# Optimization experiments

Hardware: AMD Instinct MI355X
Metric: run time of the kernel (lower is better)

## Reference

```python
import jax, jax.numpy as jnp
import numpy as np
import math

IN_CH, OUT_CH, RANK, MODES, HEAD, BATCH = 64, 64, 8, 8192, 4, 32


def setup_inputs() -> dict:
    key = jax.random.key(0)
    kx, k1, k2, k3 = jax.random.split(key, 4)
    scale = 1.0 / math.sqrt(IN_CH * OUT_CH)
    x = jax.random.normal(kx, (BATCH, IN_CH, MODES), dtype=jnp.float32)
    # Note: in the torch module, self.U1 has in_channels rows and is used as the
    # FIRST contraction ('irkh'), while self.U2 has out_channels rows and is the
    # LAST ('oskh') — the jit'd function's arg names are swapped relative to the
    # module attributes. We name params by their role here.
    U_in = scale * jax.random.uniform(k1, (IN_CH, RANK, MODES, HEAD), dtype=jnp.float32)   # self.U1
    M = scale * jax.random.uniform(k2, (RANK, RANK, MODES, HEAD), dtype=jnp.float32)       # self.M
    U_out = scale * jax.random.uniform(k3, (OUT_CH, RANK, MODES, HEAD), dtype=jnp.float32) # self.U2
    return {"x": x, "U_in": U_in, "M": M, "U_out": U_out}


def reference(x, U_in, M, U_out):
    # x: [b, i, k] -> r: [b, r, k, h]
    r = jnp.einsum('irkh,bik->brkh', U_in, x)
    # mix ranks per (mode, head): [b, s, k, h]
    s = jnp.einsum('rskh,brkh->bskh', M, r)
    # project to out channels, sum over heads: [b, o, k]
    out = jnp.einsum('oskh,bskh->bok', U_out, s)
    return out
```

## Files before the change

### kernel.cpp

```cpp
#include <hip/hip_runtime.h>


static constexpr int IN_CH  = 64;
static constexpr int OUT_CH = 64;
static constexpr int RANK   = 8;
static constexpr int MODES  = 8192;
static constexpr int KT     = 16;
static constexpr int CROWS  = 64;
static constexpr int CF4    = CROWS * KT;

typedef const __attribute__((address_space(1))) void* gas_t;
typedef __attribute__((address_space(3))) void* las_t;

#define FENCE asm volatile("" ::: "memory")

__device__ __forceinline__ void fma_s4(float4& a, const float4 w, const float v) {
    a.x = fmaf(w.x, v, a.x); a.y = fmaf(w.y, v, a.y);
    a.z = fmaf(w.z, v, a.z); a.w = fmaf(w.w, v, a.w);
}
__device__ __forceinline__ void fma_44(float4& a, const float4 w, const float4 v) {
    a.x = fmaf(w.x, v.x, a.x); a.y = fmaf(w.y, v.y, a.y);
    a.z = fmaf(w.z, v.z, a.z); a.w = fmaf(w.w, v.w, a.w);
}

__device__ __forceinline__ void stage_chunk8(const float4* gbase, float4* lbuf,
                                             int wid, int lane) {
    const int sub = lane >> 4;
    const int col = lane & 15;
#pragma unroll
    for (int j = 0; j < 2; ++j) {
        const int row0 = wid * 8 + j * 4;
        const float4* src = gbase + (size_t)(row0 + sub) * MODES + col;
        float4* dst = lbuf + row0 * KT;
        __builtin_amdgcn_global_load_lds((gas_t)src, (las_t)dst, 16, 0, 0);
    }
}

__global__ __launch_bounds__(512, 4) void diag_lr_fused(
    const float*  __restrict__ x,
    const float4* __restrict__ Uin,
    const float4* __restrict__ Mw,
    const float4* __restrict__ Uout,
    float*        __restrict__ out)
{
    __shared__ float4 lds[4][CF4];

    const int t    = threadIdx.x;
    const int kk   = t & 15;
    const int b    = t >> 4;
    const int lane = t & 63;
    const int wid  = t >> 6;
    const int k0   = blockIdx.x * KT;
    const int k    = k0 + kk;

    const float4* UinB = Uin  + k0;
    const float4* MB   = Mw   + k0;
    const float4* UoB  = Uout + k0;
    const float*  xp = x   + (size_t)b * (IN_CH  * MODES) + k;
    float*        op = out + (size_t)b * (OUT_CH * MODES) + k;

#define CHUNK_PTR(cc) ((cc) < 8 ? (UinB + (size_t)(cc) * CROWS * MODES) \
                     : (cc) == 8 ? MB \
                     : (UoB + (size_t)((cc) - 9) * CROWS * MODES))

    float xa[2][8];

    stage_chunk8(CHUNK_PTR(0), &lds[0][0], wid, lane);
    FENCE;
#pragma unroll
    for (int ii = 0; ii < 8; ++ii) xa[0][ii] = xp[ii * MODES];
    FENCE;
    stage_chunk8(CHUNK_PTR(1), &lds[1][0], wid, lane);
    FENCE;

    float4 racc[RANK];
#pragma unroll
    for (int r = 0; r < RANK; ++r) racc[r] = make_float4(0.f, 0.f, 0.f, 0.f);

#pragma unroll
    for (int c = 0; c < 8; ++c) {
        asm volatile("s_waitcnt vmcnt(2)" ::: "memory");
        __builtin_amdgcn_s_barrier();
        FENCE;
        if (c < 7) {
#pragma unroll
            for (int ii = 0; ii < 8; ++ii)
                xa[(c + 1) & 1][ii] = xp[((c + 1) * 8 + ii) * MODES];
            FENCE;
        }
        stage_chunk8(CHUNK_PTR(c + 2), &lds[(c + 2) & 3][0], wid, lane);
        FENCE;
        const float4* Lb = &lds[c & 3][0];
#pragma unroll
        for (int ii = 0; ii < 8; ++ii) {
            const float xv = xa[c & 1][ii];
#pragma unroll
            for (int r = 0; r < RANK; ++r)
                fma_s4(racc[r], Lb[(ii * 8 + r) * KT + kk], xv);
        }
        FENCE;
    }

    float4 sacc[RANK];
#pragma unroll
    for (int s = 0; s < RANK; ++s) sacc[s] = make_float4(0.f, 0.f, 0.f, 0.f);
    {
        asm volatile("s_waitcnt vmcnt(2)" ::: "memory");
        __builtin_amdgcn_s_barrier();
        FENCE;
        stage_chunk8(CHUNK_PTR(10), &lds[10 & 3][0], wid, lane);
        FENCE;
        const float4* Lb = &lds[8 & 3][0];
#pragma unroll
        for (int r = 0; r < RANK; ++r)
#pragma unroll
            for (int s = 0; s < RANK; ++s)
                fma_44(sacc[s], Lb[(r * 8 + s) * KT + kk], racc[r]);
        FENCE;
    }

#pragma unroll
    for (int c = 9; c < 17; ++c) {
        if      (c == 9)  asm volatile("s_waitcnt vmcnt(2)"  ::: "memory");
        else if (c == 10) asm volatile("s_waitcnt vmcnt(10)" ::: "memory");
        else if (c == 16) asm volatile("s_waitcnt vmcnt(16)" ::: "memory");
        else              asm volatile("s_waitcnt vmcnt(18)" ::: "memory");
        __builtin_amdgcn_s_barrier();
        FENCE;
        if (c + 2 <= 16) {
            stage_chunk8(CHUNK_PTR(c + 2), &lds[(c + 2) & 3][0], wid, lane);
            FENCE;
        }
        const float4* Lb = &lds[c & 3][0];
        const int oc = c - 9;
#pragma unroll
        for (int oo = 0; oo < 8; ++oo) {
            float4 a = make_float4(0.f, 0.f, 0.f, 0.f);
#pragma unroll
            for (int s = 0; s < RANK; ++s)
                fma_44(a, Lb[(oo * 8 + s) * KT + kk], sacc[s]);
            op[(oc * 8 + oo) * MODES] = (a.x + a.y) + (a.z + a.w);
        }
        FENCE;
    }
#undef CHUNK_PTR
}

extern "C" void kernel_launch(void* const* d_in, const int* in_sizes, int n_in,
                              void* d_out, int out_size, void* d_ws, size_t ws_size,
                              hipStream_t stream) {
    const float*  x    = (const float*)d_in[0];
    const float4* Uin  = (const float4*)d_in[1];
    const float4* Mw   = (const float4*)d_in[2];
    const float4* Uout = (const float4*)d_in[3];
    float* out = (float*)d_out;

    dim3 grid(512), block(512);
    hipLaunchKernelGGL(diag_lr_fused, grid, block, 0, stream, x, Uin, Mw, Uout, out);
}
```

Measured before the change: 74.07 us.

## Split channel work across lane halves, two batches per thread to reuse LDS weights

Each thread now handles two batch rows (bs and bs+16) and half of each 8-row channel chunk, selected by lane bit 4. Every LDS weight read feeds two FMA streams, halving LDS reads per FMA. Partial rank sums from the two halves are combined with xor-16 shuffles before the rank-mixing stage, and each half then writes half of the output channels. The cost is twice the accumulator registers (r0/r1, s0/s1), which risks spills or lower occupancy under the 512x4 launch bound, plus a redundant duplicate M-stage computation in both halves.

After: 104.0 us. 1.4x slower.

```diff
diff --git a/kernel.cpp b/kernel.cpp
--- a/kernel.cpp
+++ b/kernel.cpp
@@ -47,35 +47,45 @@
 
     const int t    = threadIdx.x;
     const int kk   = t & 15;
-    const int b    = t >> 4;
+    const int half = (t >> 4) & 1;
+    const int bs   = t >> 5;
     const int lane = t & 63;
     const int wid  = t >> 6;
     const int k0   = blockIdx.x * KT;
     const int k    = k0 + kk;
+    const int h4   = half * 4;
 
     const float4* UinB = Uin  + k0;
     const float4* MB   = Mw   + k0;
     const float4* UoB  = Uout + k0;
-    const float*  xp = x   + (size_t)b * (IN_CH  * MODES) + k;
-    float*        op = out + (size_t)b * (OUT_CH * MODES) + k;
+    const float*  xp0 = x   + (size_t)bs        * (IN_CH  * MODES) + k;
+    const float*  xp1 = x   + (size_t)(bs + 16) * (IN_CH  * MODES) + k;
+    float*        op0 = out + (size_t)bs        * (OUT_CH * MODES) + k;
+    float*        op1 = out + (size_t)(bs + 16) * (OUT_CH * MODES) + k;
 
 #define CHUNK_PTR(cc) ((cc) < 8 ? (UinB + (size_t)(cc) * CROWS * MODES) \
                      : (cc) == 8 ? MB \
                      : (UoB + (size_t)((cc) - 9) * CROWS * MODES))
 
-    float xa[2][8];
+    float xa[2][4][2];
 
     stage_chunk8(CHUNK_PTR(0), &lds[0][0], wid, lane);
     FENCE;
 #pragma unroll
-    for (int ii = 0; ii < 8; ++ii) xa[0][ii] = xp[ii * MODES];
+    for (int ii = 0; ii < 4; ++ii) {
+        xa[0][ii][0] = xp0[(h4 + ii) * MODES];
+        xa[0][ii][1] = xp1[(h4 + ii) * MODES];
+    }
     FENCE;
     stage_chunk8(CHUNK_PTR(1), &lds[1][0], wid, lane);
     FENCE;
 
-    float4 racc[RANK];
+    float4 r0[RANK], r1[RANK];
 #pragma unroll
-    for (int r = 0; r < RANK; ++r) racc[r] = make_float4(0.f, 0.f, 0.f, 0.f);
+    for (int r = 0; r < RANK; ++r) {
+        r0[r] = make_float4(0.f, 0.f, 0.f, 0.f);
+        r1[r] = make_float4(0.f, 0.f, 0.f, 0.f);
+    }
 
 #pragma unroll
     for (int c = 0; c < 8; ++c) {
@@ -84,26 +94,43 @@
         FENCE;
         if (c < 7) {
 #pragma unroll
-            for (int ii = 0; ii < 8; ++ii)
-                xa[(c + 1) & 1][ii] = xp[((c + 1) * 8 + ii) * MODES];
+            for (int ii = 0; ii < 4; ++ii) {
+                xa[(c + 1) & 1][ii][0] = xp0[((c + 1) * 8 + h4 + ii) * MODES];
+                xa[(c + 1) & 1][ii][1] = xp1[((c + 1) * 8 + h4 + ii) * MODES];
+            }
             FENCE;
         }
         stage_chunk8(CHUNK_PTR(c + 2), &lds[(c + 2) & 3][0], wid, lane);
         FENCE;
         const float4* Lb = &lds[c & 3][0];
 #pragma unroll
-        for (int ii = 0; ii < 8; ++ii) {
-            const float xv = xa[c & 1][ii];
+        for (int ii = 0; ii < 4; ++ii) {
+            const float xv0 = xa[c & 1][ii][0];
+            const float xv1 = xa[c & 1][ii][1];
 #pragma unroll
-            for (int r = 0; r < RANK; ++r)
-                fma_s4(racc[r], Lb[(ii * 8 + r) * KT + kk], xv);
+            for (int r = 0; r < RANK; ++r) {
+                const float4 w = Lb[((h4 + ii) * 8 + r) * KT + kk];
+                fma_s4(r0[r], w, xv0);
+                fma_s4(r1[r], w, xv1);
+            }
         }
         FENCE;
     }
 
-    float4 sacc[RANK];
 #pragma unroll
-    for (int s = 0; s < RANK; ++s) sacc[s] = make_float4(0.f, 0.f, 0.f, 0.f);
+    for (int r = 0; r < RANK; ++r) {
+        r0[r].x += __shfl_xor(r0[r].x, 16); r0[r].y += __shfl_xor(r0[r].y, 16);
+        r0[r].z += __shfl_xor(r0[r].z, 16); r0[r].w += __shfl_xor(r0[r].w, 16);
+        r1[r].x += __shfl_xor(r1[r].x, 16); r1[r].y += __shfl_xor(r1[r].y, 16);
+        r1[r].z += __shfl_xor(r1[r].z, 16); r1[r].w += __shfl_xor(r1[r].w, 16);
+    }
+
+    float4 s0[RANK], s1[RANK];
+#pragma unroll
+    for (int s = 0; s < RANK; ++s) {
+        s0[s] = make_float4(0.f, 0.f, 0.f, 0.f);
+        s1[s] = make_float4(0.f, 0.f, 0.f, 0.f);
+    }
     {
         asm volatile("s_waitcnt vmcnt(2)" ::: "memory");
         __builtin_amdgcn_s_barrier();
@@ -114,8 +141,11 @@
 #pragma unroll
         for (int r = 0; r < RANK; ++r)
 #pragma unroll
-            for (int s = 0; s < RANK; ++s)
-                fma_44(sacc[s], Lb[(r * 8 + s) * KT + kk], racc[r]);
+            for (int s = 0; s < RANK; ++s) {
+                const float4 w = Lb[(r * 8 + s) * KT + kk];
+                fma_44(s0[s], w, r0[r]);
+                fma_44(s1[s], w, r1[r]);
+            }
         FENCE;
     }
 
@@ -134,12 +164,18 @@
         const float4* Lb = &lds[c & 3][0];
         const int oc = c - 9;
 #pragma unroll
-        for (int oo = 0; oo < 8; ++oo) {
-            float4 a = make_float4(0.f, 0.f, 0.f, 0.f);
+        for (int oo = 0; oo < 4; ++oo) {
+            float4 a0 = make_float4(0.f, 0.f, 0.f, 0.f);
+            float4 a1 = make_float4(0.f, 0.f, 0.f, 0.f);
 #pragma unroll
-            for (int s = 0; s < RANK; ++s)
-                fma_44(a, Lb[(oo * 8 + s) * KT + kk], sacc[s]);
-            op[(oc * 8 + oo) * MODES] = (a.x + a.y) + (a.z + a.w);
+            for (int s = 0; s < RANK; ++s) {
+                const float4 w = Lb[((h4 + oo) * 8 + s) * KT + kk];
+                fma_44(a0, w, s0[s]);
+                fma_44(a1, w, s1[s]);
+            }
+            const int o = oc * 8 + h4 + oo;
+            op0[o * MODES] = (a0.x + a0.y) + (a0.z + a0.w);
+            op1[o * MODES] = (a1.x + a1.y) + (a1.z + a1.w);
         }
         FENCE;
     }
```

## Split heads across lane pairs, each thread handling two batches

Applied to the files above, without the earlier changes.

Each thread now covers two of the four heads (float2) for two batches (b and b+16), where before it covered all four heads for one batch. This halves the LDS weight reads per FMA, since each loaded float2 weight is reused for two batches. The cost is extra cross-lane shuffles to exchange x values and to reduce partial head sums before the store. Register usage per thread stays about the same, and the shuffles and select logic add some overhead.

Result: slower. 94.11 us (+27.1%).

```diff
diff --git a/kernel.cpp b/kernel.cpp
--- a/kernel.cpp
+++ b/kernel.cpp
@@ -13,15 +13,6 @@
 typedef __attribute__((address_space(3))) void* las_t;
 
 #define FENCE asm volatile("" ::: "memory")
-
-__device__ __forceinline__ void fma_s4(float4& a, const float4 w, const float v) {
-    a.x = fmaf(w.x, v, a.x); a.y = fmaf(w.y, v, a.y);
-    a.z = fmaf(w.z, v, a.z); a.w = fmaf(w.w, v, a.w);
-}
-__device__ __forceinline__ void fma_44(float4& a, const float4 w, const float4 v) {
-    a.x = fmaf(w.x, v.x, a.x); a.y = fmaf(w.y, v.y, a.y);
-    a.z = fmaf(w.z, v.z, a.z); a.w = fmaf(w.w, v.w, a.w);
-}
 
 __device__ __forceinline__ void stage_chunk8(const float4* gbase, float4* lbuf,
                                              int wid, int lane) {
@@ -47,17 +38,19 @@
 
     const int t    = threadIdx.x;
     const int kk   = t & 15;
-    const int b    = t >> 4;
+    const int hp   = (t >> 4) & 1;
+    const int bs   = t >> 5;
     const int lane = t & 63;
     const int wid  = t >> 6;
     const int k0   = blockIdx.x * KT;
     const int k    = k0 + kk;
+    const int myb  = hp ? (bs + 16) : bs;
 
     const float4* UinB = Uin  + k0;
     const float4* MB   = Mw   + k0;
     const float4* UoB  = Uout + k0;
-    const float*  xp = x   + (size_t)b * (IN_CH  * MODES) + k;
-    float*        op = out + (size_t)b * (OUT_CH * MODES) + k;
+    const float*  xp = x   + (size_t)myb * (IN_CH  * MODES) + k;
+    float*        op = out + (size_t)myb * (OUT_CH * MODES) + k;
 
 #define CHUNK_PTR(cc) ((cc) < 8 ? (UinB + (size_t)(cc) * CROWS * MODES) \
                      : (cc) == 8 ? MB \
@@ -73,9 +66,12 @@
     stage_chunk8(CHUNK_PTR(1), &lds[1][0], wid, lane);
     FENCE;
 
-    float4 racc[RANK];
+    float2 rl[RANK], rh[RANK];
 #pragma unroll
-    for (int r = 0; r < RANK; ++r) racc[r] = make_float4(0.f, 0.f, 0.f, 0.f);
+    for (int r = 0; r < RANK; ++r) {
+        rl[r] = make_float2(0.f, 0.f);
+        rh[r] = make_float2(0.f, 0.f);
+    }
 
 #pragma unroll
     for (int c = 0; c < 8; ++c) {
@@ -90,32 +86,54 @@
         }
         stage_chunk8(CHUNK_PTR(c + 2), &lds[(c + 2) & 3][0], wid, lane);
         FENCE;
-        const float4* Lb = &lds[c & 3][0];
+        const float2* Lb2 = (const float2*)&lds[c & 3][0];
 #pragma unroll
         for (int ii = 0; ii < 8; ++ii) {
-            const float xv = xa[c & 1][ii];
+            const float myx = xa[c & 1][ii];
+            const float ox  = __shfl_xor(myx, 16);
+            const float xlo = hp ? ox : myx;
+            const float xhi = hp ? myx : ox;
 #pragma unroll
-            for (int r = 0; r < RANK; ++r)
-                fma_s4(racc[r], Lb[(ii * 8 + r) * KT + kk], xv);
+            for (int r = 0; r < RANK; ++r) {
+                const float2 w = Lb2[((ii * 8 + r) * KT + kk) * 2 + hp];
+                rl[r].x = fmaf(w.x, xlo, rl[r].x);
+                rl[r].y = fmaf(w.y, xlo, rl[r].y);
+                rh[r].x = fmaf(w.x, xhi, rh[r].x);
+                rh[r].y = fmaf(w.y, xhi, rh[r].y);
+            }
         }
         FENCE;
     }
 
-    float4 sacc[RANK];
-#pragma unroll
-    for (int s = 0; s < RANK; ++s) sacc[s] = make_float4(0.f, 0.f, 0.f, 0.f);
+    float2 sl[RANK], sh[RANK];
     {
         asm volatile("s_waitcnt vmcnt(2)" ::: "memory");
         __builtin_amdgcn_s_barrier();
         FENCE;
         stage_chunk8(CHUNK_PTR(10), &lds[10 & 3][0], wid, lane);
         FENCE;
-        const float4* Lb = &lds[8 & 3][0];
+        const float2* Lb2 = (const float2*)&lds[8 & 3][0];
+#pragma unroll
+        for (int s = 0; s < RANK; ++s) sl[s] = make_float2(0.f, 0.f);
 #pragma unroll
         for (int r = 0; r < RANK; ++r)
 #pragma unroll
-            for (int s = 0; s < RANK; ++s)
-                fma_44(sacc[s], Lb[(r * 8 + s) * KT + kk], racc[r]);
+            for (int s = 0; s < RANK; ++s) {
+                const float2 w = Lb2[((r * 8 + s) * KT + kk) * 2 + hp];
+                sl[s].x = fmaf(w.x, rl[r].x, sl[s].x);
+                sl[s].y = fmaf(w.y, rl[r].y, sl[s].y);
+            }
+        FENCE;
+#pragma unroll
+        for (int s = 0; s < RANK; ++s) sh[s] = make_float2(0.f, 0.f);
+#pragma unroll
+        for (int r = 0; r < RANK; ++r)
+#pragma unroll
+            for (int s = 0; s < RANK; ++s) {
+                const float2 w = Lb2[((r * 8 + s) * KT + kk) * 2 + hp];
+                sh[s].x = fmaf(w.x, rh[r].x, sh[s].x);
+                sh[s].y = fmaf(w.y, rh[r].y, sh[s].y);
+            }
         FENCE;
     }
 
@@ -131,15 +149,25 @@
             stage_chunk8(CHUNK_PTR(c + 2), &lds[(c + 2) & 3][0], wid, lane);
             FENCE;
         }
-        const float4* Lb = &lds[c & 3][0];
+        const float2* Lb2 = (const float2*)&lds[c & 3][0];
         const int oc = c - 9;
 #pragma unroll
         for (int oo = 0; oo < 8; ++oo) {
-            float4 a = make_float4(0.f, 0.f, 0.f, 0.f);
+            float2 pl = make_float2(0.f, 0.f);
+            float2 ph = make_float2(0.f, 0.f);
 #pragma unroll
-            for (int s = 0; s < RANK; ++s)
-                fma_44(a, Lb[(oo * 8 + s) * KT + kk], sacc[s]);
-            op[(oc * 8 + oo) * MODES] = (a.x + a.y) + (a.z + a.w);
+            for (int s = 0; s < RANK; ++s) {
+                const float2 w = Lb2[((oo * 8 + s) * KT + kk) * 2 + hp];
+                pl.x = fmaf(w.x, sl[s].x, pl.x);
+                pl.y = fmaf(w.y, sl[s].y, pl.y);
+                ph.x = fmaf(w.x, sh[s].x, ph.x);
+                ph.y = fmaf(w.y, sh[s].y, ph.y);
+            }
+            float fl = pl.x + pl.y;
+            float fh = ph.x + ph.y;
+            fl += __shfl_xor(fl, 16);
+            fh += __shfl_xor(fh, 16);
+            op[(oc * 8 + oo) * MODES] = hp ? fh : fl;
         }
         FENCE;
     }
```

## Split each batch row across two thread halves with shuffle reductions, 1024-thread blocks

Applied to the files above, without the earlier changes.

Doubles the block to 1024 threads so that each (batch, mode) pair is handled by two threads. Each half processes half of the input channels, half of the rank outputs and half of the output channels. Partial r and s results are combined with cross-lane shuffles, and each staging call now issues one async global-to-LDS load per thread instead of two. The aim is more wavefronts per block to hide memory latency and fewer registers per thread, at the cost of shuffle overhead and duplicated x and weight reads.

Result: slower. 82.80 us (+11.8%).

```diff
diff --git a/kernel.cpp b/kernel.cpp
--- a/kernel.cpp
+++ b/kernel.cpp
@@ -23,20 +23,16 @@
     a.z = fmaf(w.z, v.z, a.z); a.w = fmaf(w.w, v.w, a.w);
 }
 
-__device__ __forceinline__ void stage_chunk8(const float4* gbase, float4* lbuf,
-                                             int wid, int lane) {
+__device__ __forceinline__ void stage_chunk16(const float4* gbase, float4* lbuf,
+                                              int wid, int lane) {
     const int sub = lane >> 4;
     const int col = lane & 15;
-#pragma unroll
-    for (int j = 0; j < 2; ++j) {
-        const int row0 = wid * 8 + j * 4;
-        const float4* src = gbase + (size_t)(row0 + sub) * MODES + col;
-        float4* dst = lbuf + row0 * KT;
-        __builtin_amdgcn_global_load_lds((gas_t)src, (las_t)dst, 16, 0, 0);
-    }
+    const float4* src = gbase + (size_t)(wid * 4 + sub) * MODES + col;
+    float4* dst = lbuf + wid * 4 * KT;
+    __builtin_amdgcn_global_load_lds((gas_t)src, (las_t)dst, 16, 0, 0);
 }
 
-__global__ __launch_bounds__(512, 4) void diag_lr_fused(
+__global__ __launch_bounds__(1024, 2) void diag_lr_fused(
     const float*  __restrict__ x,
     const float4* __restrict__ Uin,
     const float4* __restrict__ Mw,
@@ -47,11 +43,13 @@
 
     const int t    = threadIdx.x;
     const int kk   = t & 15;
-    const int b    = t >> 4;
+    const int half = (t >> 4) & 1;
+    const int b    = t >> 5;
     const int lane = t & 63;
     const int wid  = t >> 6;
     const int k0   = blockIdx.x * KT;
     const int k    = k0 + kk;
+    const int h4   = half * 4;
 
     const float4* UinB = Uin  + k0;
     const float4* MB   = Mw   + k0;
@@ -63,14 +61,14 @@
                      : (cc) == 8 ? MB \
                      : (UoB + (size_t)((cc) - 9) * CROWS * MODES))
 
-    float xa[2][8];
+    float xa[2][4];
 
-    stage_chunk8(CHUNK_PTR(0), &lds[0][0], wid, lane);
+    stage_chunk16(CHUNK_PTR(0), &lds[0][0], wid, lane);
     FENCE;
 #pragma unroll
-    for (int ii = 0; ii < 8; ++ii) xa[0][ii] = xp[ii * MODES];
+    for (int ii = 0; ii < 4; ++ii) xa[0][ii] = xp[(h4 + ii) * MODES];
     FENCE;
-    stage_chunk8(CHUNK_PTR(1), &lds[1][0], wid, lane);
+    stage_chunk16(CHUNK_PTR(1), &lds[1][0], wid, lane);
     FENCE;
 
     float4 racc[RANK];
@@ -79,67 +77,88 @@
 
 #pragma unroll
     for (int c = 0; c < 8; ++c) {
-        asm volatile("s_waitcnt vmcnt(2)" ::: "memory");
+        asm volatile("s_waitcnt vmcnt(1)" ::: "memory");
         __builtin_amdgcn_s_barrier();
         FENCE;
         if (c < 7) {
 #pragma unroll
-            for (int ii = 0; ii < 8; ++ii)
-                xa[(c + 1) & 1][ii] = xp[((c + 1) * 8 + ii) * MODES];
+            for (int ii = 0; ii < 4; ++ii)
+                xa[(c + 1) & 1][ii] = xp[((c + 1) * 8 + h4 + ii) * MODES];
             FENCE;
         }
-        stage_chunk8(CHUNK_PTR(c + 2), &lds[(c + 2) & 3][0], wid, lane);
+        stage_chunk16(CHUNK_PTR(c + 2), &lds[(c + 2) & 3][0], wid, lane);
         FENCE;
         const float4* Lb = &lds[c & 3][0];
 #pragma unroll
-        for (int ii = 0; ii < 8; ++ii) {
+        for (int ii = 0; ii < 4; ++ii) {
             const float xv = xa[c & 1][ii];
 #pragma unroll
             for (int r = 0; r < RANK; ++r)
-                fma_s4(racc[r], Lb[(ii * 8 + r) * KT + kk], xv);
+                fma_s4(racc[r], Lb[((h4 + ii) * 8 + r) * KT + kk], xv);
         }
         FENCE;
     }
 
-    float4 sacc[RANK];
 #pragma unroll
-    for (int s = 0; s < RANK; ++s) sacc[s] = make_float4(0.f, 0.f, 0.f, 0.f);
+    for (int r = 0; r < RANK; ++r) {
+        racc[r].x += __shfl_xor(racc[r].x, 16);
+        racc[r].y += __shfl_xor(racc[r].y, 16);
+        racc[r].z += __shfl_xor(racc[r].z, 16);
+        racc[r].w += __shfl_xor(racc[r].w, 16);
+    }
+
+    float4 sh2[4];
+#pragma unroll
+    for (int ss = 0; ss < 4; ++ss) sh2[ss] = make_float4(0.f, 0.f, 0.f, 0.f);
     {
-        asm volatile("s_waitcnt vmcnt(2)" ::: "memory");
+        asm volatile("s_waitcnt vmcnt(1)" ::: "memory");
         __builtin_amdgcn_s_barrier();
         FENCE;
-        stage_chunk8(CHUNK_PTR(10), &lds[10 & 3][0], wid, lane);
+        stage_chunk16(CHUNK_PTR(10), &lds[10 & 3][0], wid, lane);
         FENCE;
         const float4* Lb = &lds[8 & 3][0];
 #pragma unroll
         for (int r = 0; r < RANK; ++r)
 #pragma unroll
-            for (int s = 0; s < RANK; ++s)
-                fma_44(sacc[s], Lb[(r * 8 + s) * KT + kk], racc[r]);
+            for (int ss = 0; ss < 4; ++ss)
+                fma_44(sh2[ss], Lb[(r * 8 + h4 + ss) * KT + kk], racc[r]);
         FENCE;
+    }
+
+    float4 sf[RANK];
+#pragma unroll
+    for (int ss = 0; ss < 4; ++ss) {
+        const float4 mine = sh2[ss];
+        float4 oth;
+        oth.x = __shfl_xor(mine.x, 16);
+        oth.y = __shfl_xor(mine.y, 16);
+        oth.z = __shfl_xor(mine.z, 16);
+        oth.w = __shfl_xor(mine.w, 16);
+        sf[ss]     = half ? oth  : mine;
+        sf[ss + 4] = half ? mine : oth;
     }
 
 #pragma unroll
     for (int c = 9; c < 17; ++c) {
-        if      (c == 9)  asm volatile("s_waitcnt vmcnt(2)"  ::: "memory");
-        else if (c == 10) asm volatile("s_waitcnt vmcnt(10)" ::: "memory");
-        else if (c == 16) asm volatile("s_waitcnt vmcnt(16)" ::: "memory");
-        else              asm volatile("s_waitcnt vmcnt(18)" ::: "memory");
+        if      (c == 9)  asm volatile("s_waitcnt vmcnt(1)" ::: "memory");
+        else if (c == 10) asm volatile("s_waitcnt vmcnt(5)" ::: "memory");
+        else if (c == 16) asm volatile("s_waitcnt vmcnt(8)" ::: "memory");
+        else              asm volatile("s_waitcnt vmcnt(9)" ::: "memory");
         __builtin_amdgcn_s_barrier();
         FENCE;
         if (c + 2 <= 16) {
-            stage_chunk8(CHUNK_PTR(c + 2), &lds[(c + 2) & 3][0], wid, lane);
+            stage_chunk16(CHUNK_PTR(c + 2), &lds[(c + 2) & 3][0], wid, lane);
             FENCE;
         }
         const float4* Lb = &lds[c & 3][0];
         const int oc = c - 9;
 #pragma unroll
-        for (int oo = 0; oo < 8; ++oo) {
+        for (int j = 0; j < 4; ++j) {
             float4 a = make_float4(0.f, 0.f, 0.f, 0.f);
 #pragma unroll
-            for (int s = 0; s < RANK; ++s)
-                fma_44(a, Lb[(oo * 8 + s) * KT + kk], sacc[s]);
-            op[(oc * 8 + oo) * MODES] = (a.x + a.y) + (a.z + a.w);
+            for (int ss = 0; ss < RANK; ++ss)
+                fma_44(a, Lb[((h4 + j) * 8 + ss) * KT + kk], sf[ss]);
+            op[(oc * 8 + h4 + j) * MODES] = (a.x + a.y) + (a.z + a.w);
         }
         FENCE;
     }
@@ -155,6 +174,6 @@
     const float4* Uout = (const float4*)d_in[3];
     float* out = (float*)d_out;
 
-    dim3 grid(512), block(512);
+    dim3 grid(512), block(1024);
     hipLaunchKernelGGL(diag_lr_fused, grid, block, 0, stream, x, Uin, Mw, Uout, out);
 }
```
